# Kernel optimization log

Hardware: AMD Instinct MI355X
Metric: run time of the kernel (lower is better)

The kernel has to match this reference:

```python
import jax, jax.numpy as jnp
import numpy as np

T_B = 0.9  # GIoU threshold from __init__ default
EPS_ADJ = 1e-6
EPS_DEN = 1e-6


def cxcywh_to_xyxy(b):
    cx, cy, w, h = jnp.split(b, 4, axis=-1)
    return jnp.concatenate([cx - 0.5 * w, cy - 0.5 * h, cx + 0.5 * w, cy + 0.5 * h], axis=-1)


def pairwise_giou(boxes):
    # boxes: [N, 4] xyxy -> [N, N] generalized IoU (torchvision/DETR box_ops semantics)
    area = (boxes[:, 2] - boxes[:, 0]) * (boxes[:, 3] - boxes[:, 1])  # [N]
    lt = jnp.maximum(boxes[:, None, :2], boxes[None, :, :2])  # [N, N, 2]
    rb = jnp.minimum(boxes[:, None, 2:], boxes[None, :, 2:])
    wh = jnp.clip(rb - lt, 0.0)
    inter = wh[..., 0] * wh[..., 1]                            # [N, N]
    union = area[:, None] + area[None, :] - inter
    iou = inter / union
    # smallest enclosing box
    lt_e = jnp.minimum(boxes[:, None, :2], boxes[None, :, :2])
    rb_e = jnp.maximum(boxes[:, None, 2:], boxes[None, :, 2:])
    wh_e = jnp.clip(rb_e - lt_e, 0.0)
    area_e = wh_e[..., 0] * wh_e[..., 1]
    return iou - (area_e - union) / area_e


def transitive_closure(adj, n_q):
    # Fixed-point iteration: adj <- (adj + adj @ adj > 1e-6), at most n_q steps.
    # Diagonal is 1 (self-GIoU == 1 > t_b), so this converges in O(log n_q) steps.
    def cond(state):
        t, _, changed = state
        return jnp.logical_and(t < n_q, changed)

    def body(state):
        t, a, _ = state
        new = ((a + jnp.matmul(a, a)) > EPS_ADJ).astype(jnp.float32)
        return (t + 1, new, jnp.any(new != a))

    _, adj, _ = jax.lax.while_loop(cond, body, (jnp.int32(0), adj, jnp.array(True)))
    return adj


def setup_inputs() -> dict:
    key = jax.random.key(0)
    k1, k2 = jax.random.split(key)
    bboxes = jax.random.uniform(k1, (32, 900, 4), dtype=jnp.float32)
    logits = jax.random.normal(k2, (32, 900, 91), dtype=jnp.float32)
    return {"bboxes": bboxes, "logits": logits}


def reference(bboxes, logits):
    n_q = bboxes.shape[1]
    xyxy = cxcywh_to_xyxy(bboxes)                 # [B, N, 4]
    giou = jax.vmap(pairwise_giou)(xyxy)          # [B, N, N]
    mask = giou > T_B
    mask = mask | jnp.swapaxes(mask, 1, 2)        # symmetrize
    adj = transitive_closure(mask.astype(jnp.float32), n_q)  # [B, N, N]
    denom = jnp.sum(adj, axis=-1, keepdims=True) + EPS_DEN   # [B, N, 1]
    aggregated_bboxes = jnp.matmul(adj, bboxes) / denom       # [B, N, 4]
    return (aggregated_bboxes, logits, adj)
```

## Files before the change

### kernel.cpp

```cpp
#include <hip/hip_runtime.h>
#include <stdint.h>

#define NQ 900
#define NB 32
#define WORDS 16
#define ROWS_PER_BLK 30

#define AGG_ELE   0
#define LOG_ELE   115200
#define ADJ_ELE   2736000

__global__ __launch_bounds__(256) void k_mask(const float4* __restrict__ bb,
                                              unsigned long long* __restrict__ bits)
{
#pragma clang fp contract(off)
    __shared__ float sx1[NQ], sy1[NQ], sx2[NQ], sy2[NQ], sar[NQ];
    const int blk   = blockIdx.x;
    const int b     = blk / (NQ / ROWS_PER_BLK);
    const int chunk = blk % (NQ / ROWS_PER_BLK);
    const int row0  = chunk * ROWS_PER_BLK;
    const int tid   = threadIdx.x;

    for (int i = tid; i < NQ; i += 256) {
        float4 q = bb[b * NQ + i];
        float cx = q.x, cy = q.y, w = q.z, h = q.w;
        float hw = 0.5f * w, hh = 0.5f * h;
        float x1 = cx - hw, y1 = cy - hh, x2 = cx + hw, y2 = cy + hh;
        sx1[i] = x1; sy1[i] = y1; sx2[i] = x2; sy2[i] = y2;
        sar[i] = (x2 - x1) * (y2 - y1);
    }
    __syncthreads();

    const int wave = tid >> 6, lane = tid & 63;
    for (int r = row0; r < row0 + ROWS_PER_BLK; ++r) {
        float x1i = sx1[r], y1i = sy1[r], x2i = sx2[r], y2i = sy2[r], ai = sar[r];
        unsigned long long* rowp = bits + (size_t)(b * NQ + r) * WORDS;
        for (int t = 0; t < 4; ++t) {
            int word  = wave + 4 * t;
            int jbase = word << 6;
            if (jbase + 64 <= r) {
                if (lane == 0) rowp[word] = 0ULL;
                continue;
            }
            int j = jbase + lane;
            bool pred = false;
            if (j >= r && j < NQ) {
                float x1j = sx1[j], y1j = sy1[j], x2j = sx2[j], y2j = sy2[j], aj = sar[j];
                float ltx = fmaxf(x1i, x1j), lty = fmaxf(y1i, y1j);
                float rbx = fminf(x2i, x2j), rby = fminf(y2i, y2j);
                float iw  = fmaxf(rbx - ltx, 0.0f), ih = fmaxf(rby - lty, 0.0f);
                float inter = iw * ih;
                float uni   = ai + aj - inter;
                float iou   = inter / uni;
                float ex1 = fminf(x1i, x1j), ey1 = fminf(y1i, y1j);
                float ex2 = fmaxf(x2i, x2j), ey2 = fmaxf(y2i, y2j);
                float ew  = fmaxf(ex2 - ex1, 0.0f), eh2 = fmaxf(ey2 - ey1, 0.0f);
                float ae  = ew * eh2;
                float g   = iou - (ae - uni) / ae;
                pred = (g > 0.9f);
            }
            unsigned long long m = __ballot(pred);
            if (lane == 0) rowp[word] = m;
        }
    }
}

__global__ __launch_bounds__(1024) void k_label(const unsigned long long* __restrict__ bits,
                                                const float4* __restrict__ bb,
                                                int* __restrict__ labg,
                                                float4* __restrict__ agg_out)
{
    __shared__ int   lab[NQ];
    __shared__ float scx[NQ], scy[NQ], sw[NQ], sh[NQ], scnt[NQ];
    __shared__ int   changed;
    const int b   = blockIdx.x;
    const int tid = threadIdx.x;
    const size_t base = (size_t)b * NQ;

    for (int i = tid; i < NQ; i += 1024) {
        unsigned long long selfw = bits[(base + i) * WORDS + (i >> 6)];
        bool alive = (selfw >> (i & 63)) & 1ULL;
        lab[i] = alive ? i : -1;
        scx[i] = 0.f; scy[i] = 0.f; sw[i] = 0.f; sh[i] = 0.f; scnt[i] = 0.f;
    }
    if (tid == 0) changed = 0;
    __syncthreads();

    for (int iter = 0; iter < 1024; ++iter) {
        for (int i = tid; i < NQ; i += 1024) {
            int li = lab[i];
            if (li < 0) continue;
            const unsigned long long* rowp = bits + (base + i) * WORDS;
            for (int k = i >> 6; k < 15; ++k) {
                unsigned long long w = rowp[k];
                while (w) {
                    int j = (k << 6) + __builtin_ctzll(w);
                    w &= w - 1;
                    int lj = lab[j];
                    if (lj < li)      { li = lj; changed = 1; }
                    else if (lj > li) { atomicMin(&lab[j], li); changed = 1; }
                }
            }
            if (li < lab[i]) atomicMin(&lab[i], li);
        }
        __syncthreads();
        for (int i = tid; i < NQ; i += 1024) {
            int li = lab[i];
            if (li > 0) {
                int l2 = lab[li];
                if (l2 < li) lab[i] = l2;
            }
        }
        __syncthreads();
        int done = (changed == 0);
        __syncthreads();
        if (done) break;
        if (tid == 0) changed = 0;
        __syncthreads();
    }

    for (int i = tid; i < NQ; i += 1024) {
        int li = lab[i];
        if (li >= 0) {
            float4 q = bb[base + i];
            atomicAdd(&scx[li], q.x);
            atomicAdd(&scy[li], q.y);
            atomicAdd(&sw [li], q.z);
            atomicAdd(&sh [li], q.w);
            atomicAdd(&scnt[li], 1.0f);
        }
    }
    __syncthreads();

    for (int i = tid; i < NQ; i += 1024) {
        int li = lab[i];
        labg[base + i] = li;
        float4 o;
        if (li >= 0) {
            float d = scnt[li] + 1e-6f;
            o.x = scx[li] / d; o.y = scy[li] / d;
            o.z = sw [li] / d; o.w = sh [li] / d;
        } else {
            o.x = 0.f; o.y = 0.f; o.z = 0.f; o.w = 0.f;
        }
        agg_out[base + i] = o;
    }
}

__global__ __launch_bounds__(256) void k_adj(const int* __restrict__ labg,
                                             float4* __restrict__ adj)
{
    const int row = blockIdx.x;
    const int b = row / NQ;
    const int li = labg[row];
    const int4* lj4 = (const int4*)(labg + (size_t)b * NQ);
    float4* out = adj + (size_t)row * (NQ / 4);
    for (int t = threadIdx.x; t < NQ / 4; t += 256) {
        int4 l = lj4[t];
        float4 o;
        o.x = (l.x == li && li >= 0) ? 1.0f : 0.f;
        o.y = (l.y == li && li >= 0) ? 1.0f : 0.f;
        o.z = (l.z == li && li >= 0) ? 1.0f : 0.f;
        o.w = (l.w == li && li >= 0) ? 1.0f : 0.f;
        out[t] = o;
    }
}

#define LOG_F4 655200
__global__ __launch_bounds__(256) void k_copy(const float4* __restrict__ src,
                                              float4* __restrict__ dst)
{
    int i = blockIdx.x * 256 + threadIdx.x;
    if (i < LOG_F4) dst[i] = src[i];
}

extern "C" void kernel_launch(void* const* d_in, const int* in_sizes, int n_in,
                              void* d_out, int out_size, void* d_ws, size_t ws_size,
                              hipStream_t stream) {
    (void)in_sizes; (void)n_in; (void)out_size; (void)d_ws; (void)ws_size;
    const float4* bb = (const float4*)d_in[0];
    const float4* logits = (const float4*)d_in[1];
    float* outf = (float*)d_out;

    unsigned long long* bits = (unsigned long long*)(outf + ADJ_ELE);
    int*    labg = (int*)(outf + LOG_ELE);
    float4* agg  = (float4*)(outf + AGG_ELE);
    float4* adj  = (float4*)(outf + ADJ_ELE);

    hipLaunchKernelGGL(k_mask,  dim3(NB * (NQ / ROWS_PER_BLK)), dim3(256), 0, stream, bb, bits);
    hipLaunchKernelGGL(k_label, dim3(NB), dim3(1024), 0, stream, bits, bb, labg, agg);
    hipLaunchKernelGGL(k_adj,   dim3(NB * NQ), dim3(256), 0, stream, labg, adj);
    hipLaunchKernelGGL(k_copy,  dim3((LOG_F4 + 255) / 256), dim3(256), 0, stream,
                       logits, (float4*)(outf + LOG_ELE));
}
```

Measured before the change: 197.6 us.

## Stage adjacency bitmask in LDS and fuse logits copy into mask kernel

```diff
diff --git a/kernel.cpp b/kernel.cpp
--- a/kernel.cpp
+++ b/kernel.cpp
@@ -5,17 +5,32 @@
 #define NB 32
 #define WORDS 16
 #define ROWS_PER_BLK 30
+#define MASK_BLKS (NB * (NQ / ROWS_PER_BLK))
+#define LOG_F4 655200
+#define COPY_BLKS ((LOG_F4 + 255) / 256)
 
 #define AGG_ELE   0
 #define LOG_ELE   115200
 #define ADJ_ELE   2736000
 
+#define WS_BITS_BYTES  (sizeof(unsigned long long) * NB * NQ * WORDS)
+#define WS_LABG_BYTES  (sizeof(int) * NB * NQ)
+#define WS_NEEDED      (WS_BITS_BYTES + WS_LABG_BYTES)
+
 __global__ __launch_bounds__(256) void k_mask(const float4* __restrict__ bb,
-                                              unsigned long long* __restrict__ bits)
+                                              unsigned long long* __restrict__ bits,
+                                              const float4* __restrict__ logits,
+                                              float4* __restrict__ logits_out)
 {
 #pragma clang fp contract(off)
+    const int blk = blockIdx.x;
+    if (blk >= MASK_BLKS) {
+        int i = (blk - MASK_BLKS) * 256 + threadIdx.x;
+        if (i < LOG_F4) logits_out[i] = logits[i];
+        return;
+    }
+
     __shared__ float sx1[NQ], sy1[NQ], sx2[NQ], sy2[NQ], sar[NQ];
-    const int blk   = blockIdx.x;
     const int b     = blk / (NQ / ROWS_PER_BLK);
     const int chunk = blk % (NQ / ROWS_PER_BLK);
     const int row0  = chunk * ROWS_PER_BLK;
@@ -70,6 +85,7 @@
                                                 int* __restrict__ labg,
                                                 float4* __restrict__ agg_out)
 {
+    __shared__ unsigned long long sbits[NQ * WORDS];
     __shared__ int   lab[NQ];
     __shared__ float scx[NQ], scy[NQ], sw[NQ], sh[NQ], scnt[NQ];
     __shared__ int   changed;
@@ -77,20 +93,29 @@
     const int tid = threadIdx.x;
     const size_t base = (size_t)b * NQ;
 
-    for (int i = tid; i < NQ; i += 1024) {
-        unsigned long long selfw = bits[(base + i) * WORDS + (i >> 6)];
+    {
+        const ulonglong2* src = (const ulonglong2*)(bits + base * WORDS);
+        ulonglong2* dst = (ulonglong2*)sbits;
+        for (int t = tid; t < NQ * WORDS / 2; t += 1024) dst[t] = src[t];
+    }
+    for (int i = tid; i < NQ; i += 1024) {
+        scx[i] = 0.f; scy[i] = 0.f; sw[i] = 0.f; sh[i] = 0.f; scnt[i] = 0.f;
+    }
+    if (tid == 0) changed = 0;
+    __syncthreads();
+
+    for (int i = tid; i < NQ; i += 1024) {
+        unsigned long long selfw = sbits[i * WORDS + (i >> 6)];
         bool alive = (selfw >> (i & 63)) & 1ULL;
         lab[i] = alive ? i : -1;
-        scx[i] = 0.f; scy[i] = 0.f; sw[i] = 0.f; sh[i] = 0.f; scnt[i] = 0.f;
-    }
-    if (tid == 0) changed = 0;
+    }
     __syncthreads();
 
     for (int iter = 0; iter < 1024; ++iter) {
         for (int i = tid; i < NQ; i += 1024) {
             int li = lab[i];
             if (li < 0) continue;
-            const unsigned long long* rowp = bits + (base + i) * WORDS;
+            const unsigned long long* rowp = sbits + i * WORDS;
             for (int k = i >> 6; k < 15; ++k) {
                 unsigned long long w = rowp[k];
                 while (w) {
@@ -166,7 +191,6 @@
     }
 }
 
-#define LOG_F4 655200
 __global__ __launch_bounds__(256) void k_copy(const float4* __restrict__ src,
                                               float4* __restrict__ dst)
 {
@@ -177,19 +201,29 @@
 extern "C" void kernel_launch(void* const* d_in, const int* in_sizes, int n_in,
                               void* d_out, int out_size, void* d_ws, size_t ws_size,
                               hipStream_t stream) {
-    (void)in_sizes; (void)n_in; (void)out_size; (void)d_ws; (void)ws_size;
+    (void)in_sizes; (void)n_in; (void)out_size;
     const float4* bb = (const float4*)d_in[0];
     const float4* logits = (const float4*)d_in[1];
     float* outf = (float*)d_out;
 
-    unsigned long long* bits = (unsigned long long*)(outf + ADJ_ELE);
-    int*    labg = (int*)(outf + LOG_ELE);
-    float4* agg  = (float4*)(outf + AGG_ELE);
-    float4* adj  = (float4*)(outf + ADJ_ELE);
-
-    hipLaunchKernelGGL(k_mask,  dim3(NB * (NQ / ROWS_PER_BLK)), dim3(256), 0, stream, bb, bits);
-    hipLaunchKernelGGL(k_label, dim3(NB), dim3(1024), 0, stream, bits, bb, labg, agg);
-    hipLaunchKernelGGL(k_adj,   dim3(NB * NQ), dim3(256), 0, stream, labg, adj);
-    hipLaunchKernelGGL(k_copy,  dim3((LOG_F4 + 255) / 256), dim3(256), 0, stream,
-                       logits, (float4*)(outf + LOG_ELE));
-}
+    float4* agg     = (float4*)(outf + AGG_ELE);
+    float4* adj     = (float4*)(outf + ADJ_ELE);
+    float4* log_out = (float4*)(outf + LOG_ELE);
+
+    if (d_ws != nullptr && ws_size >= WS_NEEDED) {
+        unsigned long long* bits = (unsigned long long*)d_ws;
+        int* labg = (int*)((char*)d_ws + WS_BITS_BYTES);
+        hipLaunchKernelGGL(k_mask,  dim3(MASK_BLKS + COPY_BLKS), dim3(256), 0, stream,
+                           bb, bits, logits, log_out);
+        hipLaunchKernelGGL(k_label, dim3(NB), dim3(1024), 0, stream, bits, bb, labg, agg);
+        hipLaunchKernelGGL(k_adj,   dim3(NB * NQ), dim3(256), 0, stream, labg, adj);
+    } else {
+        unsigned long long* bits = (unsigned long long*)(outf + ADJ_ELE);
+        int* labg = (int*)(outf + LOG_ELE);
+        hipLaunchKernelGGL(k_mask,  dim3(MASK_BLKS), dim3(256), 0, stream,
+                           bb, bits, logits, log_out);
+        hipLaunchKernelGGL(k_label, dim3(NB), dim3(1024), 0, stream, bits, bb, labg, agg);
+        hipLaunchKernelGGL(k_adj,   dim3(NB * NQ), dim3(256), 0, stream, labg, adj);
+        hipLaunchKernelGGL(k_copy,  dim3(COPY_BLKS), dim3(256), 0, stream, logits, log_out);
+    }
+}
```

After: 189.5 us. 1.04x faster.
